# Optimization experiments

Measured on AMD Instinct MI355X. Metric: run time of the kernel, lower is better.

The kernel has to match this reference:

```python
import jax, jax.numpy as jnp
import numpy as np

BLOCKS = 12
B = 2
NUM_POINTS = 100
PH = PW = 32
P = PH * PW
N = 1 + P + NUM_POINTS  # cls + patches + point tokens
SCALE = 4               # scale_method='auto' keeps last SCALE rollout layers
NUM_GT = 16
KSIZE = 11
CAM_THR = 0.2


def setup_inputs() -> dict:
    key = jax.random.key(0)
    k1, k2 = jax.random.split(key)
    attns_maps = jax.random.uniform(k1, (BLOCKS, B, N, N), dtype=jnp.float32)
    pos_inds = jax.random.randint(k2, (B, NUM_GT), 0, NUM_POINTS)
    return {"attns_maps": attns_maps, "pos_inds": pos_inds}


def _morph_close(bin_img, ksize):
    # Faithful to torch dilate()/erode(): pad with constant 0, then sliding-window
    # max (dilate) followed by pad-0 + sliding-window min (erode).
    pad = (ksize - 1) // 2
    def pool(x, init, op):
        xp = jnp.pad(x, ((0, 0), (0, 0), (pad, pad), (pad, pad)))
        return jax.lax.reduce_window(xp, init, op, (1, 1, ksize, ksize), (1, 1, 1, 1), 'VALID')
    dilated = pool(bin_img, -jnp.inf, jax.lax.max)
    eroded = pool(dilated, jnp.inf, jax.lax.min)
    return eroded


def _rollout(attns_maps):
    # multiple=True branch: residual + row-normalize, then backward rollout
    eye = jnp.eye(N, dtype=attns_maps.dtype)
    aug = attns_maps + eye
    aug = aug / aug.sum(-1, keepdims=True)
    rev = aug[::-1]  # rev[0] == aug[-1] == joint[-1]
    def step(carry, a):
        j = jnp.einsum('bij,bjk->bik', carry, a)  # joint[-i] = joint[-(i-1)] @ aug[-i]
        return j, j
    init = rev[0]
    _, rest = jax.lax.scan(step, init, rev[1:])
    joint = jnp.concatenate([init[None], rest], 0)[::-1]  # (blocks, B, N, N)
    return jnp.transpose(joint, (1, 0, 2, 3))  # (B, blocks, N, N)


def reference(attns_maps, pos_inds):
    joint = _rollout(attns_maps)[:, -SCALE:]                 # (B, S, N, N)
    pam = joint[:, :, -NUM_POINTS:, 1:1 + P]                 # (B, S, num_points, P)
    # gather matched point CAMs per image: (B, S, G, P)
    cams = jax.vmap(lambda p, idx: p[:, idx, :])(pam, pos_inds)
    cams = cams.transpose(0, 2, 1, 3).reshape(B * NUM_GT, SCALE, PH, PW)
    # per-map min-max normalization (get_bbox_from_cam_fast)
    cmin = cams.min((-2, -1), keepdims=True)
    cmax = cams.max((-2, -1), keepdims=True)
    camn = (cams - cmin) / (cmax - cmin + 1e-6)
    binm = (camn >= CAM_THR).astype(camn.dtype)
    closed = _morph_close(binm, KSIZE)                       # (M, S, H, W)
    # bbox (min_max method) over foreground of the closed mask
    fg = closed > 0.5
    xs = jnp.arange(PW, dtype=jnp.float32)
    ys = jnp.arange(PH, dtype=jnp.float32)
    col_any = fg.any(-2)  # (M, S, W)
    row_any = fg.any(-1)  # (M, S, H)
    big = jnp.float32(1e9)
    xmin = jnp.min(jnp.where(col_any, xs, big), -1)
    xmax = jnp.max(jnp.where(col_any, xs, -big), -1)
    ymin = jnp.min(jnp.where(row_any, ys, big), -1)
    ymax = jnp.max(jnp.where(row_any, ys, -big), -1)
    bbox = jnp.stack([xmin, ymin, xmax, ymax], -1)           # (M, S, 4)
    empty = ~fg.any((-2, -1))
    bbox = jnp.where(empty[..., None], jnp.array([0., 0., 1., 1.], jnp.float32), bbox)
    return camn, closed, bbox
```

## Files before the change

kernel.cpp:

```cpp
#include <hip/hip_runtime.h>

#define NBLK 12
#define BB 2
#define NPTS 100
#define PP 1024
#define NN 1125
#define NPAD 1152
#define NSCALE 4
#define NG 16
#define KPAD 5
#define CAMTHR 0.2f

#define IC_CHUNKS 25
#define ROWS_PER_CHUNK 45
#define JT_TILES 5

#define N_ROWSUM (3 * BB * NN)
#define N_INITV (BB * NG)

#define WS_ROWSUM 0
#define WS_VS (3 * BB * NPAD)
#define WS_PART (WS_VS + 4 * BB * NG * NPAD)

__device__ __forceinline__ float wave_sum(float s) {
#pragma unroll
    for (int m = 32; m > 0; m >>= 1) s += __shfl_xor(s, m, 64);
    return s;
}

__global__ void prep_kernel(const float* __restrict__ A, const int* __restrict__ pos,
                            float* __restrict__ ws) {
    int wave = threadIdx.x >> 6;
    int lane = threadIdx.x & 63;
    int task = blockIdx.x * 4 + wave;
    if (task < N_ROWSUM) {
        int i = task % NN;
        int b = (task / NN) % BB;
        int kk = task / (NN * BB);
        const float* row = A + (((size_t)(8 + kk) * BB + b) * NN + i) * NN;
        float s = 0.f;
#pragma unroll
        for (int k = 0; k < 17; ++k) s += row[lane + 64 * k];
        if (lane < NN - 17 * 64) s += row[lane + 17 * 64];
        s = wave_sum(s);
        if (lane == 0) ws[WS_ROWSUM + (kk * BB + b) * NPAD + i] = s + 1.0f;
    } else if (task < N_ROWSUM + N_INITV) {
        int t = task - N_ROWSUM;
        int g = t % NG;
        int b = t / NG;
        int r = NN - NPTS + pos[b * NG + g];
        const float* row = A + (((size_t)11 * BB + b) * NN + r) * NN;
        float s = 0.f;
#pragma unroll
        for (int k = 0; k < 17; ++k) s += row[lane + 64 * k];
        if (lane < NN - 17 * 64) s += row[lane + 17 * 64];
        s = wave_sum(s);
        float inv = 1.0f / (s + 1.0f);
        float* v = ws + WS_VS + ((3 * BB + b) * NG + g) * NPAD;
        for (int j = lane; j < NN; j += 64)
            v[j] = (row[j] + (j == r ? 1.0f : 0.0f)) * inv;
    }
}

__global__ void stage_partial_kernel(const float* __restrict__ A, float* __restrict__ ws,
                                     int blk, int kk, int s_in) {
    __shared__ float Wl[ROWS_PER_CHUNK * NG];
    int x = blockIdx.x;
    int jt = x % JT_TILES;
    int b = (x / JT_TILES) % BB;
    int ic = x / (JT_TILES * BB);
    int i0 = ic * ROWS_PER_CHUNK;
    const float* rs = ws + WS_ROWSUM + (kk * BB + b) * NPAD;
    const float* vin = ws + WS_VS + ((s_in * BB + b) * NG) * NPAD;
    for (int idx = threadIdx.x; idx < ROWS_PER_CHUNK * NG; idx += 256) {
        int il = idx / NG;
        int g = idx % NG;
        Wl[idx] = vin[g * NPAD + i0 + il] / rs[i0 + il];
    }
    __syncthreads();
    int j = jt * 256 + threadIdx.x;
    if (j < NN) {
        float acc[NG];
#pragma unroll
        for (int g = 0; g < NG; ++g) acc[g] = 0.f;
        const float* Ab = A + (((size_t)blk * BB + b) * NN + i0) * NN + j;
#pragma unroll 5
        for (int il = 0; il < ROWS_PER_CHUNK; ++il) {
            float a = Ab[(size_t)il * NN];
            const float* wrow = &Wl[il * NG];
#pragma unroll
            for (int g = 0; g < NG; ++g) acc[g] += wrow[g] * a;
        }
        float* po = ws + WS_PART + ((ic * BB + b) * NG) * NPAD + j;
#pragma unroll
        for (int g = 0; g < NG; ++g) po[(size_t)g * NPAD] = acc[g];
    }
}

__global__ void stage_reduce_kernel(float* __restrict__ ws, int kk, int s_in, int s_out) {
    int t = blockIdx.x * 256 + threadIdx.x;
    int j = t % NPAD;
    int g = (t / NPAD) % NG;
    int b = t / (NPAD * NG);
    if (b >= BB || j >= NN) return;
    float s = ws[WS_VS + ((s_in * BB + b) * NG + g) * NPAD + j]
            / ws[WS_ROWSUM + (kk * BB + b) * NPAD + j];
#pragma unroll
    for (int ic = 0; ic < IC_CHUNKS; ++ic)
        s += ws[WS_PART + ((ic * BB + b) * NG + g) * NPAD + j];
    ws[WS_VS + ((s_out * BB + b) * NG + g) * NPAD + j] = s;
}

__global__ void post_kernel(const float* __restrict__ ws, float* __restrict__ out) {
    __shared__ float redA[1024];
    __shared__ float redB[1024];
    __shared__ float img[1024];
    __shared__ float tmp[1024];
    int idx = blockIdx.x;
    int s = idx % NSCALE;
    int g = (idx / NSCALE) % NG;
    int b = idx / (NSCALE * NG);
    int p = threadIdx.x;
    float cam = ws[WS_VS + ((s * BB + b) * NG + g) * NPAD + 1 + p];
    redA[p] = cam;
    redB[p] = cam;
    __syncthreads();
    for (int st = 512; st > 0; st >>= 1) {
        if (p < st) {
            redA[p] = fminf(redA[p], redA[p + st]);
            redB[p] = fmaxf(redB[p], redB[p + st]);
        }
        __syncthreads();
    }
    float mn = redA[0], mx = redB[0];
    float camn = (cam - mn) / (mx - mn + 1e-6f);
    out[(size_t)idx * PP + p] = camn;
    float bin = camn >= CAMTHR ? 1.0f : 0.0f;
    __syncthreads();
    img[p] = bin;
    __syncthreads();
    int y = p >> 5, x = p & 31;
    float m = 0.f;
    for (int dx = -KPAD; dx <= KPAD; ++dx) {
        int xx = x + dx;
        if (xx >= 0 && xx < 32) m = fmaxf(m, img[(y << 5) | xx]);
    }
    tmp[p] = m;
    __syncthreads();
    m = 0.f;
    for (int dy = -KPAD; dy <= KPAD; ++dy) {
        int yy = y + dy;
        if (yy >= 0 && yy < 32) m = fmaxf(m, tmp[(yy << 5) | x]);
    }
    __syncthreads();
    img[p] = m;
    __syncthreads();
    float e;
    if (x < KPAD || x > 31 - KPAD) {
        e = 0.f;
    } else {
        e = 1e30f;
        for (int dx = -KPAD; dx <= KPAD; ++dx) e = fminf(e, img[(y << 5) | (x + dx)]);
    }
    tmp[p] = e;
    __syncthreads();
    float ev;
    if (y < KPAD || y > 31 - KPAD) {
        ev = 0.f;
    } else {
        ev = 1e30f;
        for (int dy = -KPAD; dy <= KPAD; ++dy) ev = fminf(ev, tmp[((y + dy) << 5) | x]);
    }
    out[(size_t)(BB * NG * NSCALE) * PP + (size_t)idx * PP + p] = ev;
    bool fg = ev > 0.5f;
    redA[p] = fg ? (float)x : 1e9f;
    redB[p] = fg ? (float)x : -1e9f;
    __syncthreads();
    for (int st = 512; st > 0; st >>= 1) {
        if (p < st) {
            redA[p] = fminf(redA[p], redA[p + st]);
            redB[p] = fmaxf(redB[p], redB[p + st]);
        }
        __syncthreads();
    }
    float xmin = redA[0], xmax = redB[0];
    __syncthreads();
    redA[p] = fg ? (float)y : 1e9f;
    redB[p] = fg ? (float)y : -1e9f;
    __syncthreads();
    for (int st = 512; st > 0; st >>= 1) {
        if (p < st) {
            redA[p] = fminf(redA[p], redA[p + st]);
            redB[p] = fmaxf(redB[p], redB[p + st]);
        }
        __syncthreads();
    }
    if (p == 0) {
        float ymin = redA[0], ymax = redB[0];
        float* bb = out + (size_t)(BB * NG * NSCALE) * PP * 2 + (size_t)idx * 4;
        if (xmax < -1e8f) {
            bb[0] = 0.f; bb[1] = 0.f; bb[2] = 1.f; bb[3] = 1.f;
        } else {
            bb[0] = xmin; bb[1] = ymin; bb[2] = xmax; bb[3] = ymax;
        }
    }
}

extern "C" void kernel_launch(void* const* d_in, const int* in_sizes, int n_in,
                              void* d_out, int out_size, void* d_ws, size_t ws_size,
                              hipStream_t stream) {
    const float* A = (const float*)d_in[0];
    const int* pos = (const int*)d_in[1];
    float* out = (float*)d_out;
    float* ws = (float*)d_ws;

    int prep_blocks = (N_ROWSUM + N_INITV + 3) / 4;
    prep_kernel<<<prep_blocks, 256, 0, stream>>>(A, pos, ws);
    for (int t = 1; t <= 3; ++t) {
        int blk = 11 - t;
        int kk = blk - 8;
        int s_in = 4 - t;
        int s_out = 3 - t;
        stage_partial_kernel<<<IC_CHUNKS * BB * JT_TILES, 256, 0, stream>>>(A, ws, blk, kk, s_in);
        stage_reduce_kernel<<<(BB * NG * NPAD + 255) / 256, 256, 0, stream>>>(ws, kk, s_in, s_out);
    }
    post_kernel<<<BB * NG * NSCALE, 1024, 0, stream>>>(ws, out);
}
```

Measured before the change: 49.98 us.

## Fuse stage reduction into next stage's weight load and drop reduce kernels

Removes the three separate reduce kernels by having each stage kernel sum the previous stage's per-chunk partials while building its shared weight tile, writing the reduced vector out once. The residual identity term is folded into the partial kernel via the diagonal, and the last reduction moves into the post kernel. Row chunks shrink from 45 to 25 rows, giving 45 chunks and more blocks. This cuts launches and round trips, but each block now redundantly re-reads 45 partials for its weight rows, and partial buffers grow.

```diff
diff --git a/kernel.cpp b/kernel.cpp
--- a/kernel.cpp
+++ b/kernel.cpp
@@ -1,6 +1,5 @@
 #include <hip/hip_runtime.h>
 
-#define NBLK 12
 #define BB 2
 #define NPTS 100
 #define PP 1024
@@ -11,16 +10,20 @@
 #define KPAD 5
 #define CAMTHR 0.2f
 
-#define IC_CHUNKS 25
-#define ROWS_PER_CHUNK 45
-#define JT_TILES 5
+#define R 25
+#define IC 45
+#define JT 5
+#define PSTRIDE (BB * NG * NPAD)
+#define PSZ (IC * PSTRIDE)
 
 #define N_ROWSUM (3 * BB * NN)
 #define N_INITV (BB * NG)
 
 #define WS_ROWSUM 0
 #define WS_VS (3 * BB * NPAD)
-#define WS_PART (WS_VS + 4 * BB * NG * NPAD)
+#define WS_P0 (WS_VS + 4 * BB * NG * NPAD)
+#define WS_P1 (WS_P0 + PSZ)
+#define WS_P2 (WS_P1 + PSZ)
 
 __device__ __forceinline__ float wave_sum(float s) {
 #pragma unroll
@@ -28,8 +31,9 @@
     return s;
 }
 
-__global__ void prep_kernel(const float* __restrict__ A, const int* __restrict__ pos,
-                            float* __restrict__ ws) {
+__global__ __launch_bounds__(256) void prep_kernel(const float* __restrict__ A,
+                                                   const int* __restrict__ pos,
+                                                   float* __restrict__ ws) {
     int wave = threadIdx.x >> 6;
     int lane = threadIdx.x & 63;
     int task = blockIdx.x * 4 + wave;
@@ -56,62 +60,65 @@
         if (lane < NN - 17 * 64) s += row[lane + 17 * 64];
         s = wave_sum(s);
         float inv = 1.0f / (s + 1.0f);
-        float* v = ws + WS_VS + ((3 * BB + b) * NG + g) * NPAD;
+        float* v = ws + WS_VS + ((size_t)(3 * BB + b) * NG + g) * NPAD;
         for (int j = lane; j < NN; j += 64)
             v[j] = (row[j] + (j == r ? 1.0f : 0.0f)) * inv;
     }
 }
 
-__global__ void stage_partial_kernel(const float* __restrict__ A, float* __restrict__ ws,
-                                     int blk, int kk, int s_in) {
-    __shared__ float Wl[ROWS_PER_CHUNK * NG];
+__global__ __launch_bounds__(256) void stage_kernel(
+        const float* __restrict__ A, const float* __restrict__ rsb,
+        const float* __restrict__ vin, const float* __restrict__ prevP,
+        float* __restrict__ curP, float* __restrict__ vout, int blk) {
+    __shared__ float Wl[R * NG];
     int x = blockIdx.x;
-    int jt = x % JT_TILES;
-    int b = (x / JT_TILES) % BB;
-    int ic = x / (JT_TILES * BB);
-    int i0 = ic * ROWS_PER_CHUNK;
-    const float* rs = ws + WS_ROWSUM + (kk * BB + b) * NPAD;
-    const float* vin = ws + WS_VS + ((s_in * BB + b) * NG) * NPAD;
-    for (int idx = threadIdx.x; idx < ROWS_PER_CHUNK * NG; idx += 256) {
-        int il = idx / NG;
-        int g = idx % NG;
-        Wl[idx] = vin[g * NPAD + i0 + il] / rs[i0 + il];
+    int jt = x % JT;
+    int b = (x / JT) % BB;
+    int ic = x / (JT * BB);
+    int i0 = ic * R;
+    const float* rs = rsb + b * NPAD;
+    for (int idx = threadIdx.x; idx < R * NG; idx += 256) {
+        int il = idx >> 4;
+        int g = idx & 15;
+        size_t voff = (size_t)(b * NG + g) * NPAD + i0 + il;
+        float v;
+        if (prevP) {
+            float s = 0.f;
+            const float* pp = prevP + voff;
+#pragma unroll
+            for (int c = 0; c < IC; ++c) s += pp[(size_t)c * PSTRIDE];
+            v = s;
+            if (vout) vout[voff] = v;
+        } else {
+            v = vin[voff];
+        }
+        Wl[idx] = v / rs[i0 + il];
     }
     __syncthreads();
     int j = jt * 256 + threadIdx.x;
-    if (j < NN) {
-        float acc[NG];
-#pragma unroll
-        for (int g = 0; g < NG; ++g) acc[g] = 0.f;
-        const float* Ab = A + (((size_t)blk * BB + b) * NN + i0) * NN + j;
-#pragma unroll 5
-        for (int il = 0; il < ROWS_PER_CHUNK; ++il) {
-            float a = Ab[(size_t)il * NN];
-            const float* wrow = &Wl[il * NG];
-#pragma unroll
-            for (int g = 0; g < NG; ++g) acc[g] += wrow[g] * a;
-        }
-        float* po = ws + WS_PART + ((ic * BB + b) * NG) * NPAD + j;
-#pragma unroll
-        for (int g = 0; g < NG; ++g) po[(size_t)g * NPAD] = acc[g];
-    }
-}
-
-__global__ void stage_reduce_kernel(float* __restrict__ ws, int kk, int s_in, int s_out) {
-    int t = blockIdx.x * 256 + threadIdx.x;
-    int j = t % NPAD;
-    int g = (t / NPAD) % NG;
-    int b = t / (NPAD * NG);
-    if (b >= BB || j >= NN) return;
-    float s = ws[WS_VS + ((s_in * BB + b) * NG + g) * NPAD + j]
-            / ws[WS_ROWSUM + (kk * BB + b) * NPAD + j];
-#pragma unroll
-    for (int ic = 0; ic < IC_CHUNKS; ++ic)
-        s += ws[WS_PART + ((ic * BB + b) * NG + g) * NPAD + j];
-    ws[WS_VS + ((s_out * BB + b) * NG + g) * NPAD + j] = s;
-}
-
-__global__ void post_kernel(const float* __restrict__ ws, float* __restrict__ out) {
+    if (j >= NN) return;
+    float acc[NG];
+#pragma unroll
+    for (int g = 0; g < NG; ++g) acc[g] = 0.f;
+    const float* Ab = A + (((size_t)blk * BB + b) * NN + i0) * NN + j;
+#pragma unroll
+    for (int il = 0; il < R; ++il) {
+        float a = Ab[(size_t)il * NN];
+#pragma unroll
+        for (int g = 0; g < NG; ++g) acc[g] += Wl[il * NG + g] * a;
+    }
+    int d = j - i0;
+    if (d >= 0 && d < R) {
+#pragma unroll
+        for (int g = 0; g < NG; ++g) acc[g] += Wl[d * NG + g];
+    }
+    float* po = curP + (size_t)(ic * BB + b) * NG * NPAD + j;
+#pragma unroll
+    for (int g = 0; g < NG; ++g) po[(size_t)g * NPAD] = acc[g];
+}
+
+__global__ __launch_bounds__(1024) void post_kernel(const float* __restrict__ ws,
+                                                    float* __restrict__ out) {
     __shared__ float redA[1024];
     __shared__ float redB[1024];
     __shared__ float img[1024];
@@ -121,7 +128,16 @@
     int g = (idx / NSCALE) % NG;
     int b = idx / (NSCALE * NG);
     int p = threadIdx.x;
-    float cam = ws[WS_VS + ((s * BB + b) * NG + g) * NPAD + 1 + p];
+    float cam;
+    if (s == 0) {
+        const float* pp = ws + WS_P2 + (size_t)(b * NG + g) * NPAD + 1 + p;
+        float t = 0.f;
+#pragma unroll
+        for (int c = 0; c < IC; ++c) t += pp[(size_t)c * PSTRIDE];
+        cam = t;
+    } else {
+        cam = ws[WS_VS + ((size_t)(s * BB + b) * NG + g) * NPAD + 1 + p];
+    }
     redA[p] = cam;
     redB[p] = cam;
     __syncthreads();
@@ -214,15 +230,19 @@
     float* out = (float*)d_out;
     float* ws = (float*)d_ws;
 
-    int prep_blocks = (N_ROWSUM + N_INITV + 3) / 4;
-    prep_kernel<<<prep_blocks, 256, 0, stream>>>(A, pos, ws);
-    for (int t = 1; t <= 3; ++t) {
-        int blk = 11 - t;
-        int kk = blk - 8;
-        int s_in = 4 - t;
-        int s_out = 3 - t;
-        stage_partial_kernel<<<IC_CHUNKS * BB * JT_TILES, 256, 0, stream>>>(A, ws, blk, kk, s_in);
-        stage_reduce_kernel<<<(BB * NG * NPAD + 255) / 256, 256, 0, stream>>>(ws, kk, s_in, s_out);
-    }
+    const float* rs2 = ws + WS_ROWSUM + 2 * BB * NPAD;
+    const float* rs1 = ws + WS_ROWSUM + 1 * BB * NPAD;
+    const float* rs0 = ws + WS_ROWSUM + 0 * BB * NPAD;
+    float* VS3 = ws + WS_VS + 3 * BB * NG * NPAD;
+    float* VS2 = ws + WS_VS + 2 * BB * NG * NPAD;
+    float* VS1 = ws + WS_VS + 1 * BB * NG * NPAD;
+
+    prep_kernel<<<(N_ROWSUM + N_INITV + 3) / 4, 256, 0, stream>>>(A, pos, ws);
+    stage_kernel<<<IC * BB * JT, 256, 0, stream>>>(A, rs2, VS3, nullptr,
+                                                   ws + WS_P0, nullptr, 10);
+    stage_kernel<<<IC * BB * JT, 256, 0, stream>>>(A, rs1, nullptr, ws + WS_P0,
+                                                   ws + WS_P1, VS2, 9);
+    stage_kernel<<<IC * BB * JT, 256, 0, stream>>>(A, rs0, nullptr, ws + WS_P1,
+                                                   ws + WS_P2, VS1, 8);
     post_kernel<<<BB * NG * NSCALE, 1024, 0, stream>>>(ws, out);
 }
```

Result: slower. 76.40 us (+52.9%).
